# Performance work log

Hardware: AMD Instinct MI355X
Metric: run time of the kernel (lower is better)

Reference implementation:

```python
import jax, jax.numpy as jnp
import numpy as np

N = 20000   # nodes
E = 160000  # edges
G = 32      # graphs in the batch
IN_DIM, HID, OUT = 27, 512, 256


def _linear_init(key, fan_in, fan_out):
    s = 1.0 / np.sqrt(fan_in)
    return jax.random.uniform(key, (fan_in, fan_out), jnp.float32, -s, s)


def setup_inputs() -> dict:
    key = jax.random.key(0)
    ks = jax.random.split(key, 16)
    feature = jax.random.normal(ks[0], (N, IN_DIM), jnp.float32)
    edge_src = jax.random.randint(ks[1], (E,), 0, N, jnp.int32)
    edge_dst = jax.random.randint(ks[2], (E,), 0, N, jnp.int32)
    graph_ids = jnp.sort(jax.random.randint(ks[3], (N,), 0, G, jnp.int32))
    dims = [(IN_DIM, HID), (HID, HID), (HID, OUT)]
    inp = {
        "feature": feature,
        "edge_src": edge_src,
        "edge_dst": edge_dst,
        "graph_ids": graph_ids,
    }
    k = 4
    for l, (fi, fo) in enumerate(dims):
        inp[f"W_self{l}"] = _linear_init(ks[k], fi, fo); k += 1
        inp[f"W_neigh{l}"] = _linear_init(ks[k], fi, fo); k += 1
        inp[f"b{l}"] = jnp.zeros((fo,), jnp.float32)
    return inp


def _sage_layer(h, edge_src, edge_dst, inv_deg, W_self, W_neigh, b):
    # mean aggregation of in-neighbors (src -> dst), DGL SAGEConv 'mean'
    msg = h[edge_src]                                   # [E, F]
    agg = jax.ops.segment_sum(msg, edge_dst, num_segments=N) * inv_deg  # [N, F]
    return h @ W_self + agg @ W_neigh + b


def reference(feature, edge_src, edge_dst, graph_ids,
              W_self0, W_neigh0, b0,
              W_self1, W_neigh1, b1,
              W_self2, W_neigh2, b2):
    ones_e = jnp.ones((E,), jnp.float32)
    deg = jax.ops.segment_sum(ones_e, edge_dst, num_segments=N)
    inv_deg = (1.0 / jnp.maximum(deg, 1.0))[:, None]    # [N, 1]

    h = _sage_layer(feature, edge_src, edge_dst, inv_deg, W_self0, W_neigh0, b0)
    h = jax.nn.relu(h)
    h = _sage_layer(h, edge_src, edge_dst, inv_deg, W_self1, W_neigh1, b1)
    h = jax.nn.relu(h)
    h = _sage_layer(h, edge_src, edge_dst, inv_deg, W_self2, W_neigh2, b2)
    # last layer: no activation (encoding=False -> last_activation=None)

    # AvgPooling: per-graph mean of node features
    ones_n = jnp.ones((N,), jnp.float32)
    counts = jax.ops.segment_sum(ones_n, graph_ids, num_segments=G)
    hg = jax.ops.segment_sum(h, graph_ids, num_segments=G) / jnp.maximum(counts, 1.0)[:, None]
    return h, hg
```

## Files before the change

### kernel.cpp

```cpp
#include <hip/hip_runtime.h>

constexpr int NN   = 20000;
constexpr int NE   = 160000;
constexpr int NG   = 32;
constexpr int IN   = 27;
constexpr int HID  = 512;
constexpr int OUT  = 256;
constexpr int MPAD = 20096;
constexpr int MT   = MPAD / 128;

typedef unsigned short u16;
typedef __bf16 bf16x8 __attribute__((ext_vector_type(8)));
typedef float  f32x4  __attribute__((ext_vector_type(4)));
typedef u16    u16x4  __attribute__((ext_vector_type(4)));

__device__ __forceinline__ u16 f2b(float x) {
  __bf16 h = (__bf16)x;
  return __builtin_bit_cast(u16, h);
}
__device__ __forceinline__ float b2f(u16 u) {
  __bf16 h = __builtin_bit_cast(__bf16, u);
  return (float)h;
}

#define GLOBAL_AS __attribute__((address_space(1)))
#define LDS_AS    __attribute__((address_space(3)))
__device__ __forceinline__ void gload_lds16(const void* g, void* l) {
  __builtin_amdgcn_global_load_lds((const GLOBAL_AS void*)g, (LDS_AS void*)l, 16, 0, 0);
}

__global__ void k_deg(const int* __restrict__ dst, int* __restrict__ deg) {
  int e = blockIdx.x * 256 + threadIdx.x;
  if (e < NE) atomicAdd(&deg[dst[e]], 1);
}

__global__ void k_scan(const int* __restrict__ deg, int* __restrict__ rowptr,
                       int* __restrict__ cursor, float* __restrict__ invdeg) {
  __shared__ int sd[1024];
  __shared__ int s_base;
  const int tid = threadIdx.x;
  if (tid == 0) s_base = 0;
  __syncthreads();
  for (int base = 0; base < NN; base += 1024) {
    const int i = base + tid;
    const int d = (i < NN) ? deg[i] : 0;
    sd[tid] = d;
    __syncthreads();
    for (int off = 1; off < 1024; off <<= 1) {
      int t = (tid >= off) ? sd[tid - off] : 0;
      __syncthreads();
      sd[tid] += t;
      __syncthreads();
    }
    const int incl  = sd[tid];
    const int total = s_base;
    if (i < NN) {
      const int excl = total + incl - d;
      rowptr[i] = excl;
      cursor[i] = excl;
      invdeg[i] = 1.0f / fmaxf((float)d, 1.0f);
    }
    __syncthreads();
    if (tid == 1023) s_base = total + sd[1023];
    __syncthreads();
  }
  if (tid == 0) rowptr[NN] = s_base;
}

__global__ void k_scatter(const int* __restrict__ src, const int* __restrict__ dst,
                          int* __restrict__ cursor, int* __restrict__ ssrc) {
  int e = blockIdx.x * 256 + threadIdx.x;
  if (e < NE) {
    int p = atomicAdd(&cursor[dst[e]], 1);
    ssrc[p] = src[e];
  }
}

__global__ void k_wconv(const float* __restrict__ W1, int K1,
                        const float* __restrict__ W2, int K2,
                        int Kpad, int Nout, u16* __restrict__ Bt) {
  int idx = blockIdx.x * 256 + threadIdx.x;
  if (idx >= Nout * Kpad) return;
  int n = idx / Kpad, k = idx % Kpad;
  float v = 0.0f;
  if (k < K1)            v = W1[(size_t)k * Nout + n];
  else if (k < K1 + K2)  v = W2[(size_t)(k - K1) * Nout + n];
  Bt[idx] = f2b(v);
}

__global__ void k_build_A0(const float* __restrict__ feat, const int* __restrict__ rowptr,
                           const int* __restrict__ ssrc, const float* __restrict__ invdeg,
                           u16* __restrict__ A0) {
  const int r = blockIdx.x, t = threadIdx.x;
  u16* row = A0 + (size_t)r * 64;
  if (r >= NN) { row[t] = 0; return; }
  if (t < IN) {
    row[t] = f2b(feat[(size_t)r * IN + t]);
    float s = 0.0f;
    const int e0 = rowptr[r], e1 = rowptr[r + 1];
    for (int e = e0; e < e1; ++e) s += feat[(size_t)ssrc[e] * IN + t];
    row[IN + t] = f2b(s * invdeg[r]);
  } else if (t >= 2 * IN) {
    row[t] = 0;
  }
}

__global__ void k_agg512(u16* __restrict__ A1, const int* __restrict__ rowptr,
                         const int* __restrict__ ssrc, const float* __restrict__ invdeg) {
  const int r = blockIdx.x, t = threadIdx.x;
  float a0 = 0, a1 = 0, a2 = 0, a3 = 0;
  const int e0 = rowptr[r], e1 = rowptr[r + 1];
  for (int e = e0; e < e1; ++e) {
    const u16x4 v = *(const u16x4*)(A1 + (size_t)ssrc[e] * 1024 + t * 4);
    a0 += b2f(v.x); a1 += b2f(v.y); a2 += b2f(v.z); a3 += b2f(v.w);
  }
  const float inv = invdeg[r];
  u16x4 o; o.x = f2b(a0 * inv); o.y = f2b(a1 * inv); o.z = f2b(a2 * inv); o.w = f2b(a3 * inv);
  *(u16x4*)(A1 + (size_t)r * 1024 + 512 + t * 4) = o;
}

__global__ void k_agg256(const u16* __restrict__ T2, const int* __restrict__ rowptr,
                         const int* __restrict__ ssrc, const float* __restrict__ invdeg,
                         float* __restrict__ AGG2) {
  const int r = blockIdx.x, t = threadIdx.x;
  float a0 = 0, a1 = 0, a2 = 0, a3 = 0;
  const int e0 = rowptr[r], e1 = rowptr[r + 1];
  for (int e = e0; e < e1; ++e) {
    const u16x4 v = *(const u16x4*)(T2 + (size_t)ssrc[e] * 256 + t * 4);
    a0 += b2f(v.x); a1 += b2f(v.y); a2 += b2f(v.z); a3 += b2f(v.w);
  }
  const float inv = invdeg[r];
  f32x4 o = {a0 * inv, a1 * inv, a2 * inv, a3 * inv};
  *(f32x4*)(AGG2 + (size_t)r * 256 + t * 4) = o;
}

__global__ __launch_bounds__(256) void k_gemm(
    const u16* __restrict__ A, int lda,
    const u16* __restrict__ Bt, int K,
    void* __restrict__ Out, int ldo,
    const float* __restrict__ bias,
    const float* __restrict__ addp,
    int flags) {
  __shared__ u16 As[128 * 64];
  __shared__ u16 Bs[128 * 64];
  const int tid = threadIdx.x;
  const int wid = tid >> 6, lane = tid & 63;
  const int l16 = lane & 15, lhi = lane >> 4;
  const int wr = wid >> 1, wc = wid & 1;
  const int row0 = blockIdx.x * 128, col0 = blockIdx.y * 128;

  const int tr    = tid >> 3;
  const int slot  = tid & 7;
  const int sslot = slot ^ (tr & 7);

  f32x4 acc[4][4] = {};

  for (int kt = 0; kt < K; kt += 64) {
#pragma unroll
    for (int i = 0; i < 4; ++i) {
      const int r = i * 32 + tr;
      gload_lds16(A  + (size_t)(row0 + r) * lda + kt + sslot * 8, &As[i * 2048 + wid * 512]);
      gload_lds16(Bt + (size_t)(col0 + r) * K   + kt + sslot * 8, &Bs[i * 2048 + wid * 512]);
    }
    __syncthreads();
#pragma unroll
    for (int ks = 0; ks < 2; ++ks) {
      bf16x8 af[4], bfr[4];
#pragma unroll
      for (int i = 0; i < 4; ++i) {
        const int r = wr * 64 + i * 16 + l16;
        const int s = (ks * 4 + lhi) ^ (r & 7);
        af[i] = *(const bf16x8*)&As[r * 64 + s * 8];
      }
#pragma unroll
      for (int n = 0; n < 4; ++n) {
        const int c = wc * 64 + n * 16 + l16;
        const int s = (ks * 4 + lhi) ^ (c & 7);
        bfr[n] = *(const bf16x8*)&Bs[c * 64 + s * 8];
      }
#pragma unroll
      for (int i = 0; i < 4; ++i)
#pragma unroll
        for (int n = 0; n < 4; ++n)
          acc[i][n] = __builtin_amdgcn_mfma_f32_16x16x32_bf16(af[i], bfr[n], acc[i][n], 0, 0, 0);
    }
    __syncthreads();
  }

  const bool relu = flags & 1;
  const bool f32o = flags & 2;
#pragma unroll
  for (int i = 0; i < 4; ++i) {
#pragma unroll
    for (int n = 0; n < 4; ++n) {
      const int C = col0 + wc * 64 + n * 16 + l16;
      const float bv = bias ? bias[C] : 0.0f;
#pragma unroll
      for (int q = 0; q < 4; ++q) {
        const int R = row0 + wr * 64 + i * 16 + lhi * 4 + q;
        float v = acc[i][n][q] + bv;
        if (f32o) {
          if (R < NN) {
            if (addp) v += addp[(size_t)R * ldo + C];
            ((float*)Out)[(size_t)R * ldo + C] = v;
          }
        } else {
          if (relu) v = fmaxf(v, 0.0f);
          ((u16*)Out)[(size_t)R * ldo + C] = f2b(v);
        }
      }
    }
  }
}

__global__ void k_gbounds(const int* __restrict__ gid, int* __restrict__ gstart) {
  const int g = threadIdx.x;
  if (g > NG) return;
  int lo = 0, hi = NN;
  while (lo < hi) {
    const int mid = (lo + hi) >> 1;
    if (gid[mid] < g) lo = mid + 1; else hi = mid;
  }
  gstart[g] = lo;
}
__global__ void k_pool(const float* __restrict__ h, const int* __restrict__ gstart,
                       float* __restrict__ hg) {
  const int g = blockIdx.x >> 3, s = blockIdx.x & 7;
  const int t = threadIdx.x;
  const int n0 = gstart[g], n1 = gstart[g + 1];
  const int len = n1 - n0, chunk = (len + 7) / 8;
  const int a = n0 + s * chunk;
  const int b = min(a + chunk, n1);
  float acc = 0.0f;
  for (int i = a; i < b; ++i) acc += h[(size_t)i * 256 + t];
  if (b > a) atomicAdd(&hg[g * 256 + t], acc);
}
__global__ void k_pooldiv(float* __restrict__ hg, const int* __restrict__ gstart) {
  const int g = blockIdx.x, t = threadIdx.x;
  const float c = (float)(gstart[g + 1] - gstart[g]);
  hg[g * 256 + t] /= fmaxf(c, 1.0f);
}

constexpr size_t OFF_A0    = 0;
constexpr size_t OFF_A1    = OFF_A0   + (size_t)MPAD * 64  * 2;
constexpr size_t OFF_H1    = OFF_A1   + (size_t)MPAD * 1024 * 2;
constexpr size_t OFF_T2    = OFF_H1   + (size_t)MPAD * 512 * 2;
constexpr size_t OFF_AGG2  = OFF_T2   + (size_t)MPAD * 256 * 2;
constexpr size_t OFF_BT0   = OFF_AGG2 + (size_t)NN * 256 * 4;
constexpr size_t OFF_BT1   = OFF_BT0  + (size_t)512 * 64 * 2;
constexpr size_t OFF_BTS2  = OFF_BT1  + (size_t)512 * 1024 * 2;
constexpr size_t OFF_BTN2  = OFF_BTS2 + (size_t)256 * 512 * 2;
constexpr size_t OFF_DEG   = OFF_BTN2 + (size_t)256 * 512 * 2;
constexpr size_t OFF_RP    = OFF_DEG  + (size_t)NN * 4;
constexpr size_t OFF_CUR   = OFF_RP   + (size_t)(NN + 2) * 4;
constexpr size_t OFF_SSRC  = OFF_CUR  + (size_t)NN * 4;
constexpr size_t OFF_INVD  = OFF_SSRC + (size_t)NE * 4;
constexpr size_t OFF_GST   = OFF_INVD + (size_t)NN * 4;

extern "C" void kernel_launch(void* const* d_in, const int* in_sizes, int n_in,
                              void* d_out, int out_size, void* d_ws, size_t ws_size,
                              hipStream_t stream) {
  const float* feature = (const float*)d_in[0];
  const int*   esrc    = (const int*)d_in[1];
  const int*   edst    = (const int*)d_in[2];
  const int*   gid     = (const int*)d_in[3];
  const float* Ws0 = (const float*)d_in[4],  *Wn0 = (const float*)d_in[5],  *b0 = (const float*)d_in[6];
  const float* Ws1 = (const float*)d_in[7],  *Wn1 = (const float*)d_in[8],  *b1 = (const float*)d_in[9];
  const float* Ws2 = (const float*)d_in[10], *Wn2 = (const float*)d_in[11], *b2 = (const float*)d_in[12];

  char* ws = (char*)d_ws;
  u16*   A0    = (u16*)  (ws + OFF_A0);
  u16*   A1    = (u16*)  (ws + OFF_A1);
  u16*   H1    = (u16*)  (ws + OFF_H1);
  u16*   T2    = (u16*)  (ws + OFF_T2);
  float* AGG2  = (float*)(ws + OFF_AGG2);
  u16*   Bt0   = (u16*)  (ws + OFF_BT0);
  u16*   Bt1   = (u16*)  (ws + OFF_BT1);
  u16*   BtS2  = (u16*)  (ws + OFF_BTS2);
  u16*   BtN2  = (u16*)  (ws + OFF_BTN2);
  int*   deg   = (int*)  (ws + OFF_DEG);
  int*   rp    = (int*)  (ws + OFF_RP);
  int*   cur   = (int*)  (ws + OFF_CUR);
  int*   ssrc  = (int*)  (ws + OFF_SSRC);
  float* invd  = (float*)(ws + OFF_INVD);
  int*   gst   = (int*)  (ws + OFF_GST);

  float* out_h  = (float*)d_out;
  float* out_hg = out_h + (size_t)NN * OUT;

  hipMemsetAsync(deg,  0, (size_t)NN * 4, stream);
  hipMemsetAsync(out_hg, 0, (size_t)NG * OUT * 4, stream);

  k_deg    <<<(NE + 255) / 256, 256, 0, stream>>>(edst, deg);
  k_scan   <<<1, 1024, 0, stream>>>(deg, rp, cur, invd);
  k_scatter<<<(NE + 255) / 256, 256, 0, stream>>>(esrc, edst, cur, ssrc);

  k_wconv<<<(512 * 64   + 255) / 256, 256, 0, stream>>>(Ws0, IN,  Wn0, IN,  64,   512, Bt0);
  k_wconv<<<(512 * 1024 + 255) / 256, 256, 0, stream>>>(Ws1, HID, Wn1, HID, 1024, 512, Bt1);
  k_wconv<<<(256 * 512  + 255) / 256, 256, 0, stream>>>(Ws2, HID, nullptr, 0, 512, 256, BtS2);
  k_wconv<<<(256 * 512  + 255) / 256, 256, 0, stream>>>(Wn2, HID, nullptr, 0, 512, 256, BtN2);

  k_build_A0<<<MPAD, 64, 0, stream>>>(feature, rp, ssrc, invd, A0);
  k_gemm<<<dim3(MT, 4), 256, 0, stream>>>(A0, 64, Bt0, 64, A1, 1024, b0, nullptr, 1);

  k_agg512<<<NN, 128, 0, stream>>>(A1, rp, ssrc, invd);
  k_gemm<<<dim3(MT, 4), 256, 0, stream>>>(A1, 1024, Bt1, 1024, H1, 512, b1, nullptr, 1);

  k_gemm<<<dim3(MT, 2), 256, 0, stream>>>(H1, 512, BtN2, 512, T2, 256, nullptr, nullptr, 0);
  k_agg256<<<NN, 64, 0, stream>>>(T2, rp, ssrc, invd, AGG2);
  k_gemm<<<dim3(MT, 2), 256, 0, stream>>>(H1, 512, BtS2, 512, out_h, 256, b2, AGG2, 2);

  k_gbounds<<<1, 64, 0, stream>>>(gid, gst);
  k_pool   <<<NG * 8, 256, 0, stream>>>(out_h, gst, out_hg);
  k_pooldiv<<<NG, 256, 0, stream>>>(out_hg, gst);
}
```

Before: 345.3 us.

## Rewrite degree scan as single-pass wave scan and merge small setup kernels

The prefix scan over node degrees changes from a 20-pass LDS Hillis-Steele loop with many barriers to a per-thread serial chunk plus a wave shuffle scan and a 16-entry cross-wave combine. The four weight conversion launches are merged into one kernel. The graph-bounds kernel is removed and each pooling block does its own binary search instead. The aim is fewer launches and less serialized time in single-block kernels, at the cost of repeated binary searches and strided per-thread degree loads.

```diff
diff --git a/kernel.cpp b/kernel.cpp
--- a/kernel.cpp
+++ b/kernel.cpp
@@ -36,35 +36,47 @@
 
 __global__ void k_scan(const int* __restrict__ deg, int* __restrict__ rowptr,
                        int* __restrict__ cursor, float* __restrict__ invdeg) {
-  __shared__ int sd[1024];
-  __shared__ int s_base;
+  constexpr int CH = 20;
+  __shared__ int wsum[16];
   const int tid = threadIdx.x;
-  if (tid == 0) s_base = 0;
+  const int i0 = tid * CH;
+  int loc[CH];
+  int sum = 0;
+#pragma unroll
+  for (int j = 0; j < CH; ++j) {
+    const int i = i0 + j;
+    loc[j] = sum;
+    sum += (i < NN) ? deg[i] : 0;
+  }
+  const int lane = tid & 63, wv = tid >> 6;
+  int incl = sum;
+#pragma unroll
+  for (int off = 1; off < 64; off <<= 1) {
+    int n = __shfl_up(incl, off);
+    if (lane >= off) incl += n;
+  }
+  if (lane == 63) wsum[wv] = incl;
   __syncthreads();
-  for (int base = 0; base < NN; base += 1024) {
-    const int i = base + tid;
-    const int d = (i < NN) ? deg[i] : 0;
-    sd[tid] = d;
-    __syncthreads();
-    for (int off = 1; off < 1024; off <<= 1) {
-      int t = (tid >= off) ? sd[tid - off] : 0;
-      __syncthreads();
-      sd[tid] += t;
-      __syncthreads();
-    }
-    const int incl  = sd[tid];
-    const int total = s_base;
+  if (tid == 0) {
+    int s = 0;
+#pragma unroll
+    for (int w = 0; w < 16; ++w) { int v = wsum[w]; wsum[w] = s + v; s += v; }
+  }
+  __syncthreads();
+  const int wbase = (wv == 0) ? 0 : wsum[wv - 1];
+  const int tbase = wbase + incl - sum;
+#pragma unroll
+  for (int j = 0; j < CH; ++j) {
+    const int i = i0 + j;
     if (i < NN) {
-      const int excl = total + incl - d;
+      const int excl = tbase + loc[j];
+      const int d = ((j + 1 < CH) ? loc[j + 1] : sum) - loc[j];
       rowptr[i] = excl;
       cursor[i] = excl;
       invdeg[i] = 1.0f / fmaxf((float)d, 1.0f);
     }
-    __syncthreads();
-    if (tid == 1023) s_base = total + sd[1023];
-    __syncthreads();
-  }
-  if (tid == 0) rowptr[NN] = s_base;
+  }
+  if (tid == 0) rowptr[NN] = wsum[15];
 }
 
 __global__ void k_scatter(const int* __restrict__ src, const int* __restrict__ dst,
@@ -76,16 +88,42 @@
   }
 }
 
-__global__ void k_wconv(const float* __restrict__ W1, int K1,
-                        const float* __restrict__ W2, int K2,
-                        int Kpad, int Nout, u16* __restrict__ Bt) {
+constexpr int WC0 = 512 * 64;
+constexpr int WC1 = 512 * 1024;
+constexpr int WC2 = 256 * 512;
+constexpr int WCT = WC0 + WC1 + 2 * WC2;
+__global__ void k_wconv_all(const float* __restrict__ Ws0, const float* __restrict__ Wn0,
+                            const float* __restrict__ Ws1, const float* __restrict__ Wn1,
+                            const float* __restrict__ Ws2, const float* __restrict__ Wn2,
+                            u16* __restrict__ Bt0, u16* __restrict__ Bt1,
+                            u16* __restrict__ BtS2, u16* __restrict__ BtN2) {
   int idx = blockIdx.x * 256 + threadIdx.x;
-  if (idx >= Nout * Kpad) return;
-  int n = idx / Kpad, k = idx % Kpad;
-  float v = 0.0f;
-  if (k < K1)            v = W1[(size_t)k * Nout + n];
-  else if (k < K1 + K2)  v = W2[(size_t)(k - K1) * Nout + n];
-  Bt[idx] = f2b(v);
+  if (idx < WC0) {
+    const int n = idx / 64, k = idx % 64;
+    float v = 0.0f;
+    if (k < IN)           v = Ws0[(size_t)k * 512 + n];
+    else if (k < 2 * IN)  v = Wn0[(size_t)(k - IN) * 512 + n];
+    Bt0[idx] = f2b(v);
+    return;
+  }
+  idx -= WC0;
+  if (idx < WC1) {
+    const int n = idx / 1024, k = idx % 1024;
+    const float v = (k < 512) ? Ws1[(size_t)k * 512 + n] : Wn1[(size_t)(k - 512) * 512 + n];
+    Bt1[idx] = f2b(v);
+    return;
+  }
+  idx -= WC1;
+  if (idx < WC2) {
+    const int n = idx / 512, k = idx % 512;
+    BtS2[idx] = f2b(Ws2[(size_t)k * 256 + n]);
+    return;
+  }
+  idx -= WC2;
+  if (idx < WC2) {
+    const int n = idx / 512, k = idx % 512;
+    BtN2[idx] = f2b(Wn2[(size_t)k * 256 + n]);
+  }
 }
 
 __global__ void k_build_A0(const float* __restrict__ feat, const int* __restrict__ rowptr,
@@ -213,21 +251,22 @@
   }
 }
 
-__global__ void k_gbounds(const int* __restrict__ gid, int* __restrict__ gstart) {
-  const int g = threadIdx.x;
-  if (g > NG) return;
+__device__ __forceinline__ int lower_bound_g(const int* __restrict__ gid, int g) {
   int lo = 0, hi = NN;
   while (lo < hi) {
     const int mid = (lo + hi) >> 1;
     if (gid[mid] < g) lo = mid + 1; else hi = mid;
   }
-  gstart[g] = lo;
-}
-__global__ void k_pool(const float* __restrict__ h, const int* __restrict__ gstart,
+  return lo;
+}
+__global__ void k_pool(const float* __restrict__ h, const int* __restrict__ gid,
                        float* __restrict__ hg) {
+  __shared__ int s_n0, s_n1;
   const int g = blockIdx.x >> 3, s = blockIdx.x & 7;
   const int t = threadIdx.x;
-  const int n0 = gstart[g], n1 = gstart[g + 1];
+  if (t == 0) { s_n0 = lower_bound_g(gid, g); s_n1 = lower_bound_g(gid, g + 1); }
+  __syncthreads();
+  const int n0 = s_n0, n1 = s_n1;
   const int len = n1 - n0, chunk = (len + 7) / 8;
   const int a = n0 + s * chunk;
   const int b = min(a + chunk, n1);
@@ -235,10 +274,12 @@
   for (int i = a; i < b; ++i) acc += h[(size_t)i * 256 + t];
   if (b > a) atomicAdd(&hg[g * 256 + t], acc);
 }
-__global__ void k_pooldiv(float* __restrict__ hg, const int* __restrict__ gstart) {
+__global__ void k_pooldiv(float* __restrict__ hg, const int* __restrict__ gid) {
+  __shared__ int s_c;
   const int g = blockIdx.x, t = threadIdx.x;
-  const float c = (float)(gstart[g + 1] - gstart[g]);
-  hg[g * 256 + t] /= fmaxf(c, 1.0f);
+  if (t == 0) s_c = lower_bound_g(gid, g + 1) - lower_bound_g(gid, g);
+  __syncthreads();
+  hg[g * 256 + t] /= fmaxf((float)s_c, 1.0f);
 }
 
 constexpr size_t OFF_A0    = 0;
@@ -255,7 +296,6 @@
 constexpr size_t OFF_CUR   = OFF_RP   + (size_t)(NN + 2) * 4;
 constexpr size_t OFF_SSRC  = OFF_CUR  + (size_t)NN * 4;
 constexpr size_t OFF_INVD  = OFF_SSRC + (size_t)NE * 4;
-constexpr size_t OFF_GST   = OFF_INVD + (size_t)NN * 4;
 
 extern "C" void kernel_launch(void* const* d_in, const int* in_sizes, int n_in,
                               void* d_out, int out_size, void* d_ws, size_t ws_size,
@@ -283,7 +323,6 @@
   int*   cur   = (int*)  (ws + OFF_CUR);
   int*   ssrc  = (int*)  (ws + OFF_SSRC);
   float* invd  = (float*)(ws + OFF_INVD);
-  int*   gst   = (int*)  (ws + OFF_GST);
 
   float* out_h  = (float*)d_out;
   float* out_hg = out_h + (size_t)NN * OUT;
@@ -295,10 +334,8 @@
   k_scan   <<<1, 1024, 0, stream>>>(deg, rp, cur, invd);
   k_scatter<<<(NE + 255) / 256, 256, 0, stream>>>(esrc, edst, cur, ssrc);
 
-  k_wconv<<<(512 * 64   + 255) / 256, 256, 0, stream>>>(Ws0, IN,  Wn0, IN,  64,   512, Bt0);
-  k_wconv<<<(512 * 1024 + 255) / 256, 256, 0, stream>>>(Ws1, HID, Wn1, HID, 1024, 512, Bt1);
-  k_wconv<<<(256 * 512  + 255) / 256, 256, 0, stream>>>(Ws2, HID, nullptr, 0, 512, 256, BtS2);
-  k_wconv<<<(256 * 512  + 255) / 256, 256, 0, stream>>>(Wn2, HID, nullptr, 0, 512, 256, BtN2);
+  k_wconv_all<<<(WCT + 255) / 256, 256, 0, stream>>>(Ws0, Wn0, Ws1, Wn1, Ws2, Wn2,
+                                                     Bt0, Bt1, BtS2, BtN2);
 
   k_build_A0<<<MPAD, 64, 0, stream>>>(feature, rp, ssrc, invd, A0);
   k_gemm<<<dim3(MT, 4), 256, 0, stream>>>(A0, 64, Bt0, 64, A1, 1024, b0, nullptr, 1);
@@ -310,7 +347,6 @@
   k_agg256<<<NN, 64, 0, stream>>>(T2, rp, ssrc, invd, AGG2);
   k_gemm<<<dim3(MT, 2), 256, 0, stream>>>(H1, 512, BtS2, 512, out_h, 256, b2, AGG2, 2);
 
-  k_gbounds<<<1, 64, 0, stream>>>(gid, gst);
-  k_pool   <<<NG * 8, 256, 0, stream>>>(out_h, gst, out_hg);
-  k_pooldiv<<<NG, 256, 0, stream>>>(out_hg, gst);
-}
+  k_pool   <<<NG * 8, 256, 0, stream>>>(out_h, gid, out_hg);
+  k_pooldiv<<<NG, 256, 0, stream>>>(out_hg, gid);
+}
```

Result: faster. 331.6 us (-4.0%).
